# Kernel optimization log

Measured on AMD Instinct MI355X. Metric: run time of the kernel, lower is better.

## Reference

```python
import jax, jax.numpy as jnp
import numpy as np

INPUT_DIM = 4096
HIDDEN_DIMS = [2048, 1024, 512]
OUTPUT_DIM = 2
LAYER_DIMS = [INPUT_DIM] + HIDDEN_DIMS + [OUTPUT_DIM]
LAYER_IDX = np.concatenate([[0], np.cumsum(LAYER_DIMS)]).astype(int).tolist()
TOTAL_NODES = LAYER_IDX[-1]
FAN_IN = 128
BATCH = 512
EPS = 1e-5


def setup_inputs() -> dict:
    # Layered edge topology: each node in layer i receives FAN_IN random edges
    # from layer i-1 (matches how BINN uses set_connections).
    rng = np.random.default_rng(0)
    srcs, tgts = [], []
    for i in range(1, len(LAYER_DIMS)):
        ps, pe = LAYER_IDX[i - 1], LAYER_IDX[i]
        s, e = LAYER_IDX[i], LAYER_IDX[i + 1]
        dim = e - s
        srcs.append(rng.integers(ps, pe, size=(dim, FAN_IN)).reshape(-1))
        tgts.append(np.repeat(np.arange(s, e), FAN_IN))
    edge_src = jnp.asarray(np.concatenate(srcs), jnp.int32)
    edge_tgt = jnp.asarray(np.concatenate(tgts), jnp.int32)
    E = edge_src.shape[0]

    key = jax.random.key(0)
    kx, kw = jax.random.split(key)
    x = jax.random.normal(kx, (BATCH, INPUT_DIM), jnp.float32)
    # weight = randn(E) * 1/sqrt(fan_in)  (fan_in is FAN_IN for every target)
    weight = jax.random.normal(kw, (E,), jnp.float32) * (1.0 / np.sqrt(FAN_IN))
    bias = jnp.zeros((TOTAL_NODES - INPUT_DIM,), jnp.float32)
    n_hidden = sum(HIDDEN_DIMS)
    ln_gamma = jnp.ones((n_hidden,), jnp.float32)
    ln_beta = jnp.zeros((n_hidden,), jnp.float32)
    return dict(x=x, weight=weight, bias=bias, ln_gamma=ln_gamma,
                ln_beta=ln_beta, edge_src=edge_src, edge_tgt=edge_tgt)


def reference(x, weight, bias, ln_gamma, ln_beta, edge_src, edge_tgt):
    # activations held as [total_nodes, B] so segment_sum scatters on axis 0
    B = x.shape[0]
    acts = jnp.zeros((TOTAL_NODES, B), x.dtype).at[:INPUT_DIM].set(x.T)
    n_layers = len(LAYER_DIMS)
    for i in range(1, n_layers):  # fixed small layer count
        # full sparse mm over ALL edges each layer (faithful to original)
        contrib = weight[:, None] * acts[edge_src]            # [E, B]
        ws = jax.ops.segment_sum(contrib, edge_tgt,
                                 num_segments=TOTAL_NODES)    # [N, B]
        s, e = LAYER_IDX[i], LAYER_IDX[i + 1]
        cur = ws[s:e] + bias[s - INPUT_DIM:e - INPUT_DIM, None]
        if i < n_layers - 1:
            hs, he = s - INPUT_DIM, e - INPUT_DIM
            mean = jnp.mean(cur, axis=0, keepdims=True)
            var = jnp.var(cur, axis=0, keepdims=True)  # biased, as torch LN
            cur = (ln_gamma[hs:he, None] * (cur - mean) * jax.lax.rsqrt(var + EPS)
                   + ln_beta[hs:he, None])
            cur = jax.nn.relu(cur)
        acts = acts.at[s:e].set(cur)
    return acts[LAYER_IDX[-2]:LAYER_IDX[-1]].T  # [B, output_dim]
```

## Files before the change

### kernel.cpp

```cpp
#include <hip/hip_runtime.h>

#define BATCH 512
#define FAN_IN 128
#define EPS 1e-5f

typedef unsigned short u16;
typedef unsigned int u32;
typedef _Float16 f16;
typedef __attribute__((ext_vector_type(8))) short short8;
typedef __attribute__((ext_vector_type(4))) float f32x4;
typedef __attribute__((ext_vector_type(4))) _Float16 f16x4;

__device__ __forceinline__ u16 f2bf(float f) {
    union { float f; u32 u; } v; v.f = f;
    u32 r = v.u + 0x7fffu + ((v.u >> 16) & 1u);
    return (u16)(r >> 16);
}
__device__ __forceinline__ void ld16(const void* g, void* l) {
    __builtin_amdgcn_global_load_lds(
        (const __attribute__((address_space(1))) u32*)g,
        (__attribute__((address_space(3))) u32*)l, 16, 0, 0);
}

__device__ __forceinline__ void densify_node(
    float* row, int Kin, int ebase, int srcbase, u16* outrow,
    const float* __restrict__ weight, const int* __restrict__ edge_src) {
    const int t = threadIdx.x;
    for (int k = t; k < Kin; k += 256) row[k] = 0.f;
    __syncthreads();
    if (t < FAN_IN)
        atomicAdd(&row[edge_src[ebase + t] - srcbase], weight[ebase + t]);
    __syncthreads();
    for (int k0 = t * 8; k0 < Kin; k0 += 2048) {
        u16 pk[8];
#pragma unroll
        for (int i = 0; i < 8; ++i) pk[i] = f2bf(row[k0 + i]);
        *(uint4*)(outrow + k0) = *(const uint4*)pk;
    }
}

__global__ __launch_bounds__(256) void prep(
    const float* __restrict__ weight, const int* __restrict__ edge_src,
    const float* __restrict__ x, u16* __restrict__ Wd, u16* __restrict__ xb) {
    __shared__ float row[4096];
    const int bid = blockIdx.x, t = threadIdx.x;
    if (bid < 2048) {
        densify_node(row, 4096, bid * 128, 0, Wd + (size_t)bid * 4096,
                     weight, edge_src);
    } else {
        const int b = bid - 2048;
        const float* xr = x + (size_t)b * 4096;
        u16* xo = xb + (size_t)b * 4096;
        for (int k0 = t * 8; k0 < 4096; k0 += 2048) {
            const float4 f0 = *(const float4*)(xr + k0);
            const float4 f1 = *(const float4*)(xr + k0 + 4);
            uint4 pk;
            pk.x = f2bf(f0.x) | ((u32)f2bf(f0.y) << 16);
            pk.y = f2bf(f0.z) | ((u32)f2bf(f0.w) << 16);
            pk.z = f2bf(f1.x) | ((u32)f2bf(f1.y) << 16);
            pk.w = f2bf(f1.z) | ((u32)f2bf(f1.w) << 16);
            *(uint4*)(xo + k0) = pk;
        }
    }
}

__device__ __forceinline__ void gemm_body(
    u16* SM, int m_t, int n_t, int z, const u16* __restrict__ Act,
    const u16* __restrict__ W, f16* __restrict__ Cz, int M, int K,
    int kchunk) {
    u16* sA = SM;
    u16* sB = SM + 4096;
    const int tid = threadIdx.x;
    const int m0 = m_t * 64, n0 = n_t * 64, kbase = z * kchunk;
    f16* Cp = Cz + (size_t)z * BATCH * M;

    const int r = tid >> 2, c = tid & 3;
    const int q = c ^ ((r ^ (r >> 2)) & 3);
    const u16* gA = Act + (size_t)(n0 + r) * K + kbase + q * 8;
    const u16* gB = W + (size_t)(m0 + r) * K + kbase + q * 8;
    const int lo = tid * 8;

    const int wave = tid >> 6, lane = tid & 63;
    const int l15 = lane & 15, quad = lane >> 4;
    const int aoff = (wave & 1) * 32, boff = (wave >> 1) * 32;
    int offA[2], offB[2];
#pragma unroll
    for (int i = 0; i < 2; ++i) {
        const int ra = aoff + i * 16 + l15;
        offA[i] = ra * 32 + ((quad ^ ((ra ^ (ra >> 2)) & 3)) * 8);
        const int rb = boff + i * 16 + l15;
        offB[i] = rb * 32 + ((quad ^ ((rb ^ (rb >> 2)) & 3)) * 8);
    }

    f32x4 acc[2][2] = {};
    const int niter = kchunk >> 5;
    ld16(gA, &sA[lo]); ld16(gB, &sB[lo]);
    for (int it = 0; it < niter; ++it) {
        __syncthreads();
        if (it + 1 < niter) {
            const int k0 = (it + 1) << 5;
            const int nb = ((it + 1) & 1) * 2048;
            ld16(gA + k0, &sA[nb + lo]); ld16(gB + k0, &sB[nb + lo]);
        }
        const u16* a = sA + (it & 1) * 2048;
        const u16* b = sB + (it & 1) * 2048;
        const short8 a0 = *(const short8*)(a + offA[0]);
        const short8 a1 = *(const short8*)(a + offA[1]);
        const short8 b0 = *(const short8*)(b + offB[0]);
        const short8 b1 = *(const short8*)(b + offB[1]);
        acc[0][0] = __builtin_amdgcn_mfma_f32_16x16x32_bf16(a0, b0, acc[0][0], 0, 0, 0);
        acc[0][1] = __builtin_amdgcn_mfma_f32_16x16x32_bf16(a0, b1, acc[0][1], 0, 0, 0);
        acc[1][0] = __builtin_amdgcn_mfma_f32_16x16x32_bf16(a1, b0, acc[1][0], 0, 0, 0);
        acc[1][1] = __builtin_amdgcn_mfma_f32_16x16x32_bf16(a1, b1, acc[1][1], 0, 0, 0);
    }
#pragma unroll
    for (int i = 0; i < 2; ++i) {
        const int nb = n_t * 64 + aoff + i * 16 + quad * 4;
#pragma unroll
        for (int rr = 0; rr < 4; ++rr)
#pragma unroll
            for (int j = 0; j < 2; ++j) {
                const int mg = m0 + boff + j * 16 + l15;
                Cp[(size_t)(nb + rr) * M + mg] = (f16)acc[i][j][rr];
            }
    }
}

__device__ __forceinline__ void gemm128_body(
    u16* SM, int m_t, int n_t, int z, const u16* __restrict__ Act,
    const u16* __restrict__ W, f16* __restrict__ Cz, int M, int K,
    int kchunk) {
    u16* sA = SM;
    u16* sB = SM + 8192;
    const int tid = threadIdx.x;
    const int m0 = m_t * 128, n0 = n_t * 128, kbase = z * kchunk;
    f16* Cp = Cz + (size_t)z * BATCH * M;

    const int r = tid >> 2, c = tid & 3;
    const int q1 = c ^ ((r ^ (r >> 2)) & 3);
    const int r2 = r + 64;
    const int q2 = c ^ ((r2 ^ (r2 >> 2)) & 3);
    const u16* gA1 = Act + (size_t)(n0 + r) * K + kbase + q1 * 8;
    const u16* gA2 = Act + (size_t)(n0 + r2) * K + kbase + q2 * 8;
    const u16* gB1 = W + (size_t)(m0 + r) * K + kbase + q1 * 8;
    const u16* gB2 = W + (size_t)(m0 + r2) * K + kbase + q2 * 8;
    const int lo1 = tid * 8, lo2 = tid * 8 + 2048;

    const int wave = tid >> 6, lane = tid & 63;
    const int l15 = lane & 15, quad = lane >> 4;
    const int wn = (wave & 1) * 64, wm = (wave >> 1) * 64;
    int offA[4], offB[4];
#pragma unroll
    for (int i = 0; i < 4; ++i) {
        const int na = wn + i * 16 + l15;
        offA[i] = na * 32 + ((quad ^ ((na ^ (na >> 2)) & 3)) * 8);
        const int mb = wm + i * 16 + l15;
        offB[i] = mb * 32 + ((quad ^ ((mb ^ (mb >> 2)) & 3)) * 8);
    }

    f32x4 acc[4][4] = {};
    const int niter = kchunk >> 5;
    ld16(gA1, &sA[lo1]); ld16(gA2, &sA[lo2]);
    ld16(gB1, &sB[lo1]); ld16(gB2, &sB[lo2]);
    for (int it = 0; it < niter; ++it) {
        __syncthreads();
        if (it + 1 < niter) {
            const int k0 = (it + 1) << 5;
            const int nb = ((it + 1) & 1) * 4096;
            ld16(gA1 + k0, &sA[nb + lo1]); ld16(gA2 + k0, &sA[nb + lo2]);
            ld16(gB1 + k0, &sB[nb + lo1]); ld16(gB2 + k0, &sB[nb + lo2]);
        }
        const u16* a = sA + (it & 1) * 4096;
        const u16* b = sB + (it & 1) * 4096;
        short8 av[4], bv[4];
#pragma unroll
        for (int i = 0; i < 4; ++i) av[i] = *(const short8*)(a + offA[i]);
#pragma unroll
        for (int j = 0; j < 4; ++j) bv[j] = *(const short8*)(b + offB[j]);
#pragma unroll
        for (int i = 0; i < 4; ++i)
#pragma unroll
            for (int j = 0; j < 4; ++j)
                acc[i][j] = __builtin_amdgcn_mfma_f32_16x16x32_bf16(
                    av[i], bv[j], acc[i][j], 0, 0, 0);
    }
#pragma unroll
    for (int i = 0; i < 4; ++i) {
        const int nb = n0 + wn + i * 16 + quad * 4;
#pragma unroll
        for (int rr = 0; rr < 4; ++rr)
#pragma unroll
            for (int j = 0; j < 4; ++j) {
                const int mg = m0 + wm + j * 16 + l15;
                Cp[(size_t)(nb + rr) * M + mg] = (f16)acc[i][j][rr];
            }
    }
}

__global__ __launch_bounds__(256) void g1d(
    const u16* __restrict__ xb, u16* __restrict__ Wd, f16* __restrict__ Cz1,
    const float* __restrict__ weight, const int* __restrict__ edge_src) {
    __shared__ u16 SM[16384];
    const int bid = blockIdx.x;
    if (bid < 512) {
        gemm128_body(SM, bid & 15, (bid >> 4) & 3, bid >> 6, xb, Wd, Cz1,
                     2048, 4096, 512);
    } else if (bid < 1536) {
        const int u = bid - 512;
        densify_node((float*)SM, 2048, 262144 + u * 128, 4096,
                     Wd + 8388608 + (size_t)u * 2048, weight, edge_src);
    } else {
        const int u = bid - 1536;
        densify_node((float*)SM, 1024, 393216 + u * 128, 6144,
                     Wd + 10485760 + (size_t)u * 1024, weight, edge_src);
    }
}

__global__ __launch_bounds__(256, 8) void gemm_bt(
    const u16* __restrict__ Act, const u16* __restrict__ W,
    f16* __restrict__ Cz, int M, int K, int kchunk) {
    __shared__ u16 SM[8192];
    gemm_body(SM, blockIdx.x, blockIdx.y, blockIdx.z, Act, W, Cz, M, K, kchunk);
}

template <int M, int Z, bool WOUT>
__global__ __launch_bounds__(256) void fin(
    const f16* __restrict__ Cz, const float* __restrict__ bias_l,
    const float* __restrict__ gamma_l, const float* __restrict__ beta_l,
    u16* __restrict__ actb, const float* __restrict__ weight,
    const int* __restrict__ edge_src, const float* __restrict__ obias,
    float* __restrict__ out) {
    __shared__ float rowL[M];
    __shared__ float red[8];
    __shared__ float mrs[2];
    __shared__ float w_s[256];
    __shared__ int   s_s[256];
    __shared__ float pr[256];

    const int n = blockIdx.x, t = threadIdx.x;
    const size_t zs = (size_t)BATCH * M;
    const f16* base = Cz + (size_t)n * M;

    if (WOUT) { w_s[t] = weight[458752 + t]; s_s[t] = edge_src[458752 + t] - 7168; }

    float sum = 0.f, sq = 0.f;
    for (int m = t * 4; m < M; m += 1024) {
        float4 v = *(const float4*)(bias_l + m);
#pragma unroll
        for (int z = 0; z < Z; ++z) {
            const f16x4 cv = *(const f16x4*)(base + (size_t)z * zs + m);
            v.x += (float)cv.x; v.y += (float)cv.y;
            v.z += (float)cv.z; v.w += (float)cv.w;
        }
        *(float4*)(rowL + m) = v;
        sum += v.x + v.y + v.z + v.w;
        sq += v.x * v.x + v.y * v.y + v.z * v.z + v.w * v.w;
    }
#pragma unroll
    for (int o = 32; o; o >>= 1) { sum += __shfl_down(sum, o); sq += __shfl_down(sq, o); }
    if ((t & 63) == 0) { red[(t >> 6) * 2] = sum; red[(t >> 6) * 2 + 1] = sq; }
    __syncthreads();
    if (t == 0) {
        const float s = red[0] + red[2] + red[4] + red[6];
        const float qq = red[1] + red[3] + red[5] + red[7];
        const float mean = s / (float)M;
        const float var = qq / (float)M - mean * mean;
        mrs[0] = mean; mrs[1] = rsqrtf(var + EPS);
    }
    __syncthreads();
    const float mean = mrs[0], rstd = mrs[1];

    for (int m = t * 4; m < M; m += 1024) {
        const float4 v = *(const float4*)(rowL + m);
        const float4 g = *(const float4*)(gamma_l + m);
        const float4 bt = *(const float4*)(beta_l + m);
        const float o0 = fmaxf(fmaf(g.x * (v.x - mean), rstd, bt.x), 0.f);
        const float o1 = fmaxf(fmaf(g.y * (v.y - mean), rstd, bt.y), 0.f);
        const float o2 = fmaxf(fmaf(g.z * (v.z - mean), rstd, bt.z), 0.f);
        const float o3 = fmaxf(fmaf(g.w * (v.w - mean), rstd, bt.w), 0.f);
        if (WOUT) {
            rowL[m + 0] = o0; rowL[m + 1] = o1; rowL[m + 2] = o2; rowL[m + 3] = o3;
        } else {
            u16 pk[4] = {f2bf(o0), f2bf(o1), f2bf(o2), f2bf(o3)};
            *(uint2*)(actb + (size_t)n * M + m) = *(const uint2*)pk;
        }
    }
    if (WOUT) {
        __syncthreads();
        pr[t] = w_s[t] * rowL[s_s[t]];
        __syncthreads();
        if (t < 2) {
            float s = 0.f;
            for (int k = 0; k < FAN_IN; ++k) s += pr[t * FAN_IN + k];
            out[(size_t)n * 2 + t] = s + obias[t];
        }
    }
}

extern "C" void kernel_launch(void* const* d_in, const int* in_sizes, int n_in,
                              void* d_out, int out_size, void* d_ws, size_t ws_size,
                              hipStream_t stream) {
    const float* x        = (const float*)d_in[0];
    const float* weight   = (const float*)d_in[1];
    const float* bias     = (const float*)d_in[2];
    const float* ln_gamma = (const float*)d_in[3];
    const float* ln_beta  = (const float*)d_in[4];
    const int*   edge_src = (const int*)d_in[5];
    float* out = (float*)d_out;

    f16* Cz1 = (f16*)d_ws;
    f16* Cz2 = Cz1 + (size_t)8 * 512 * 2048;
    f16* Cz3 = Cz2 + (size_t)4 * 512 * 1024;
    u16* xb    = (u16*)(Cz3 + (size_t)8 * 512 * 512);
    u16* actb1 = xb + (size_t)512 * 4096;
    u16* actb2 = actb1 + (size_t)512 * 2048;
    u16* Wd    = actb2 + (size_t)512 * 1024;

    prep<<<2560, 256, 0, stream>>>(weight, edge_src, x, Wd, xb);
    g1d<<<2048, 256, 0, stream>>>(xb, Wd, Cz1, weight, edge_src);
    fin<2048, 8, false><<<512, 256, 0, stream>>>(
        Cz1, bias, ln_gamma, ln_beta, actb1, nullptr, nullptr, nullptr, nullptr);
    gemm_bt<<<dim3(16, 8, 4), 256, 0, stream>>>(actb1, Wd + 8388608, Cz2,
                                                1024, 2048, 512);
    fin<1024, 4, false><<<512, 256, 0, stream>>>(
        Cz2, bias + 2048, ln_gamma + 2048, ln_beta + 2048, actb2,
        nullptr, nullptr, nullptr, nullptr);
    gemm_bt<<<dim3(8, 8, 8), 256, 0, stream>>>(actb2, Wd + 10485760, Cz3,
                                               512, 1024, 128);
    fin<512, 8, true><<<512, 256, 0, stream>>>(
        Cz3, bias + 3072, ln_gamma + 3072, ln_beta + 3072, nullptr,
        weight, edge_src, bias + 3584, out);
}
```

Baseline: 118.8 us.

## Replace densified GEMM pipeline with direct sparse gather and atomic LN stats

Drops per-call weight densification and dense bf16 MFMA GEMMs. Each layer now directly gathers FAN_IN source rows of a transposed bf16 activation matrix. Per-batch LayerNorm sums are accumulated with shared and global atomics, then applied in a separate kernel. The final output layer is fused with the last LN. This does far fewer FLOPs but depends on irregular gather bandwidth and on atomics.

```diff
diff --git a/kernel.cpp b/kernel.cpp
--- a/kernel.cpp
+++ b/kernel.cpp
@@ -6,295 +6,137 @@
 
 typedef unsigned short u16;
 typedef unsigned int u32;
-typedef _Float16 f16;
-typedef __attribute__((ext_vector_type(8))) short short8;
-typedef __attribute__((ext_vector_type(4))) float f32x4;
-typedef __attribute__((ext_vector_type(4))) _Float16 f16x4;
 
 __device__ __forceinline__ u16 f2bf(float f) {
     union { float f; u32 u; } v; v.f = f;
     u32 r = v.u + 0x7fffu + ((v.u >> 16) & 1u);
     return (u16)(r >> 16);
 }
-__device__ __forceinline__ void ld16(const void* g, void* l) {
-    __builtin_amdgcn_global_load_lds(
-        (const __attribute__((address_space(1))) u32*)g,
-        (__attribute__((address_space(3))) u32*)l, 16, 0, 0);
+__device__ __forceinline__ float bf2f(u16 h) {
+    union { u32 u; float f; } v; v.u = ((u32)h) << 16; return v.f;
 }
 
-__device__ __forceinline__ void densify_node(
-    float* row, int Kin, int ebase, int srcbase, u16* outrow,
-    const float* __restrict__ weight, const int* __restrict__ edge_src) {
-    const int t = threadIdx.x;
-    for (int k = t; k < Kin; k += 256) row[k] = 0.f;
+__global__ __launch_bounds__(256) void prepk(
+    const float* __restrict__ x, u16* __restrict__ xT,
+    float* __restrict__ stats) {
+    const int tid = threadIdx.x, bid = blockIdx.x;
+    if (bid == 512) {
+        for (int i = tid; i < 3072; i += 256) stats[i] = 0.f;
+        return;
+    }
+    __shared__ float T[64][65];
+    const int f0 = (bid & 63) * 64, b0 = (bid >> 6) * 64;
+    const int r = tid >> 4, c4 = (tid & 15) * 4;
+#pragma unroll
+    for (int rr = 0; rr < 4; ++rr) {
+        const int row = r + rr * 16;
+        const float4 v = *(const float4*)(x + (size_t)(b0 + row) * 4096 + f0 + c4);
+        T[row][c4] = v.x; T[row][c4 + 1] = v.y;
+        T[row][c4 + 2] = v.z; T[row][c4 + 3] = v.w;
+    }
     __syncthreads();
-    if (t < FAN_IN)
-        atomicAdd(&row[edge_src[ebase + t] - srcbase], weight[ebase + t]);
-    __syncthreads();
-    for (int k0 = t * 8; k0 < Kin; k0 += 2048) {
-        u16 pk[8];
 #pragma unroll
-        for (int i = 0; i < 8; ++i) pk[i] = f2bf(row[k0 + i]);
-        *(uint4*)(outrow + k0) = *(const uint4*)pk;
+    for (int half = 0; half < 2; ++half) {
+        const int fr = (tid >> 3) + half * 32;
+        const int bq = (tid & 7) * 8;
+        uint4 pk;
+        pk.x = (u32)f2bf(T[bq + 0][fr]) | ((u32)f2bf(T[bq + 1][fr]) << 16);
+        pk.y = (u32)f2bf(T[bq + 2][fr]) | ((u32)f2bf(T[bq + 3][fr]) << 16);
+        pk.z = (u32)f2bf(T[bq + 4][fr]) | ((u32)f2bf(T[bq + 5][fr]) << 16);
+        pk.w = (u32)f2bf(T[bq + 6][fr]) | ((u32)f2bf(T[bq + 7][fr]) << 16);
+        *(uint4*)(xT + (size_t)(f0 + fr) * 512 + b0 + bq) = pk;
     }
 }
 
-__global__ __launch_bounds__(256) void prep(
-    const float* __restrict__ weight, const int* __restrict__ edge_src,
-    const float* __restrict__ x, u16* __restrict__ Wd, u16* __restrict__ xb) {
-    __shared__ float row[4096];
-    const int bid = blockIdx.x, t = threadIdx.x;
-    if (bid < 2048) {
-        densify_node(row, 4096, bid * 128, 0, Wd + (size_t)bid * 4096,
-                     weight, edge_src);
-    } else {
-        const int b = bid - 2048;
-        const float* xr = x + (size_t)b * 4096;
-        u16* xo = xb + (size_t)b * 4096;
-        for (int k0 = t * 8; k0 < 4096; k0 += 2048) {
-            const float4 f0 = *(const float4*)(xr + k0);
-            const float4 f1 = *(const float4*)(xr + k0 + 4);
-            uint4 pk;
-            pk.x = f2bf(f0.x) | ((u32)f2bf(f0.y) << 16);
-            pk.y = f2bf(f0.z) | ((u32)f2bf(f0.w) << 16);
-            pk.z = f2bf(f1.x) | ((u32)f2bf(f1.y) << 16);
-            pk.w = f2bf(f1.z) | ((u32)f2bf(f1.w) << 16);
-            *(uint4*)(xo + k0) = pk;
-        }
+template <int NT, int EBASE, int SRCBASE>
+__global__ __launch_bounds__(256) void gatherk(
+    const u16* __restrict__ srcAct, const float* __restrict__ weight,
+    const int* __restrict__ edge_src, const float* __restrict__ bias_l,
+    float* __restrict__ raw, float* __restrict__ gcs,
+    float* __restrict__ gcq) {
+    __shared__ float cs[256];
+    __shared__ float cq[256];
+    const int tid = threadIdx.x, bid = blockIdx.x;
+    const int rr = bid & 7, kk = bid >> 3;
+    const int bc = rr >> 2;
+    const int ng = kk * 4 + (rr & 3);
+    const int wave = __builtin_amdgcn_readfirstlane(tid >> 6);
+    const int lane = tid & 63;
+    const int node = ng * 4 + wave;
+    const u16* sb = srcAct + bc * 256 + lane * 4;
+    const int ebase = EBASE + node * FAN_IN;
+    float a0 = 0.f, a1 = 0.f, a2 = 0.f, a3 = 0.f;
+#pragma unroll 8
+    for (int k = 0; k < FAN_IN; ++k) {
+        const int src = edge_src[ebase + k] - SRCBASE;
+        const float w = weight[ebase + k];
+        const ushort4 v = *(const ushort4*)(sb + (size_t)src * 512);
+        a0 = fmaf(w, bf2f(v.x), a0);
+        a1 = fmaf(w, bf2f(v.y), a1);
+        a2 = fmaf(w, bf2f(v.z), a2);
+        a3 = fmaf(w, bf2f(v.w), a3);
+    }
+    const float bv = bias_l[node];
+    a0 += bv; a1 += bv; a2 += bv; a3 += bv;
+    float4 o; o.x = a0; o.y = a1; o.z = a2; o.w = a3;
+    *(float4*)(raw + (size_t)node * 512 + bc * 256 + lane * 4) = o;
+
+    cs[tid] = 0.f; cq[tid] = 0.f;
+    __syncthreads();
+    const int lb = lane * 4;
+    atomicAdd(&cs[lb + 0], a0); atomicAdd(&cq[lb + 0], a0 * a0);
+    atomicAdd(&cs[lb + 1], a1); atomicAdd(&cq[lb + 1], a1 * a1);
+    atomicAdd(&cs[lb + 2], a2); atomicAdd(&cq[lb + 2], a2 * a2);
+    atomicAdd(&cs[lb + 3], a3); atomicAdd(&cq[lb + 3], a3 * a3);
+    __syncthreads();
+    atomicAdd(&gcs[bc * 256 + tid], cs[tid]);
+    atomicAdd(&gcq[bc * 256 + tid], cq[tid]);
+}
+
+template <int M>
+__global__ __launch_bounds__(256) void lnapplyk(
+    const float* __restrict__ raw, const float* __restrict__ gcs,
+    const float* __restrict__ gcq, const float* __restrict__ gamma_l,
+    const float* __restrict__ beta_l, u16* __restrict__ actT) {
+    const int tid = threadIdx.x;
+    const int b0 = tid * 2;
+    const float inv = 1.f / (float)M;
+    const float m0 = gcs[b0] * inv, m1 = gcs[b0 + 1] * inv;
+    const float r0 = rsqrtf(gcq[b0] * inv - m0 * m0 + EPS);
+    const float r1 = rsqrtf(gcq[b0 + 1] * inv - m1 * m1 + EPS);
+    for (int row = blockIdx.x; row < M; row += 256) {
+        const float2 v = *(const float2*)(raw + (size_t)row * 512 + b0);
+        const float g = gamma_l[row], bt = beta_l[row];
+        const float o0 = fmaxf(fmaf(g * (v.x - m0), r0, bt), 0.f);
+        const float o1 = fmaxf(fmaf(g * (v.y - m1), r1, bt), 0.f);
+        *(u32*)(actT + (size_t)row * 512 + b0) =
+            (u32)f2bf(o0) | ((u32)f2bf(o1) << 16);
     }
 }
 
-__device__ __forceinline__ void gemm_body(
-    u16* SM, int m_t, int n_t, int z, const u16* __restrict__ Act,
-    const u16* __restrict__ W, f16* __restrict__ Cz, int M, int K,
-    int kchunk) {
-    u16* sA = SM;
-    u16* sB = SM + 4096;
-    const int tid = threadIdx.x;
-    const int m0 = m_t * 64, n0 = n_t * 64, kbase = z * kchunk;
-    f16* Cp = Cz + (size_t)z * BATCH * M;
-
-    const int r = tid >> 2, c = tid & 3;
-    const int q = c ^ ((r ^ (r >> 2)) & 3);
-    const u16* gA = Act + (size_t)(n0 + r) * K + kbase + q * 8;
-    const u16* gB = W + (size_t)(m0 + r) * K + kbase + q * 8;
-    const int lo = tid * 8;
-
-    const int wave = tid >> 6, lane = tid & 63;
-    const int l15 = lane & 15, quad = lane >> 4;
-    const int aoff = (wave & 1) * 32, boff = (wave >> 1) * 32;
-    int offA[2], offB[2];
-#pragma unroll
-    for (int i = 0; i < 2; ++i) {
-        const int ra = aoff + i * 16 + l15;
-        offA[i] = ra * 32 + ((quad ^ ((ra ^ (ra >> 2)) & 3)) * 8);
-        const int rb = boff + i * 16 + l15;
-        offB[i] = rb * 32 + ((quad ^ ((rb ^ (rb >> 2)) & 3)) * 8);
+__global__ __launch_bounds__(256) void outk(
+    const float* __restrict__ raw3, const float* __restrict__ gcs,
+    const float* __restrict__ gcq, const float* __restrict__ weight,
+    const int* __restrict__ edge_src, const float* __restrict__ gamma_l,
+    const float* __restrict__ beta_l, const float* __restrict__ bias_o,
+    float* __restrict__ out) {
+    const int tid = threadIdx.x, bid = blockIdx.x;
+    const int tgt = __builtin_amdgcn_readfirstlane(tid >> 7);
+    const int b = bid * 128 + (tid & 127);
+    const float inv = 1.f / 512.f;
+    const float mb = gcs[b] * inv;
+    const float rb = rsqrtf(gcq[b] * inv - mb * mb + EPS);
+    const int ebase = 458752 + tgt * FAN_IN;
+    float acc = 0.f;
+#pragma unroll 8
+    for (int k = 0; k < FAN_IN; ++k) {
+        const int src = edge_src[ebase + k] - 7168;
+        const float w = weight[ebase + k];
+        const float g = gamma_l[src], bt = beta_l[src];
+        const float v = raw3[(size_t)src * 512 + b];
+        acc = fmaf(w, fmaxf(fmaf(g * (v - mb), rb, bt), 0.f), acc);
     }
-
-    f32x4 acc[2][2] = {};
-    const int niter = kchunk >> 5;
-    ld16(gA, &sA[lo]); ld16(gB, &sB[lo]);
-    for (int it = 0; it < niter; ++it) {
-        __syncthreads();
-        if (it + 1 < niter) {
-            const int k0 = (it + 1) << 5;
-            const int nb = ((it + 1) & 1) * 2048;
-            ld16(gA + k0, &sA[nb + lo]); ld16(gB + k0, &sB[nb + lo]);
-        }
-        const u16* a = sA + (it & 1) * 2048;
-        const u16* b = sB + (it & 1) * 2048;
-        const short8 a0 = *(const short8*)(a + offA[0]);
-        const short8 a1 = *(const short8*)(a + offA[1]);
-        const short8 b0 = *(const short8*)(b + offB[0]);
-        const short8 b1 = *(const short8*)(b + offB[1]);
-        acc[0][0] = __builtin_amdgcn_mfma_f32_16x16x32_bf16(a0, b0, acc[0][0], 0, 0, 0);
-        acc[0][1] = __builtin_amdgcn_mfma_f32_16x16x32_bf16(a0, b1, acc[0][1], 0, 0, 0);
-        acc[1][0] = __builtin_amdgcn_mfma_f32_16x16x32_bf16(a1, b0, acc[1][0], 0, 0, 0);
-        acc[1][1] = __builtin_amdgcn_mfma_f32_16x16x32_bf16(a1, b1, acc[1][1], 0, 0, 0);
-    }
-#pragma unroll
-    for (int i = 0; i < 2; ++i) {
-        const int nb = n_t * 64 + aoff + i * 16 + quad * 4;
-#pragma unroll
-        for (int rr = 0; rr < 4; ++rr)
-#pragma unroll
-            for (int j = 0; j < 2; ++j) {
-                const int mg = m0 + boff + j * 16 + l15;
-                Cp[(size_t)(nb + rr) * M + mg] = (f16)acc[i][j][rr];
-            }
-    }
-}
-
-__device__ __forceinline__ void gemm128_body(
-    u16* SM, int m_t, int n_t, int z, const u16* __restrict__ Act,
-    const u16* __restrict__ W, f16* __restrict__ Cz, int M, int K,
-    int kchunk) {
-    u16* sA = SM;
-    u16* sB = SM + 8192;
-    const int tid = threadIdx.x;
-    const int m0 = m_t * 128, n0 = n_t * 128, kbase = z * kchunk;
-    f16* Cp = Cz + (size_t)z * BATCH * M;
-
-    const int r = tid >> 2, c = tid & 3;
-    const int q1 = c ^ ((r ^ (r >> 2)) & 3);
-    const int r2 = r + 64;
-    const int q2 = c ^ ((r2 ^ (r2 >> 2)) & 3);
-    const u16* gA1 = Act + (size_t)(n0 + r) * K + kbase + q1 * 8;
-    const u16* gA2 = Act + (size_t)(n0 + r2) * K + kbase + q2 * 8;
-    const u16* gB1 = W + (size_t)(m0 + r) * K + kbase + q1 * 8;
-    const u16* gB2 = W + (size_t)(m0 + r2) * K + kbase + q2 * 8;
-    const int lo1 = tid * 8, lo2 = tid * 8 + 2048;
-
-    const int wave = tid >> 6, lane = tid & 63;
-    const int l15 = lane & 15, quad = lane >> 4;
-    const int wn = (wave & 1) * 64, wm = (wave >> 1) * 64;
-    int offA[4], offB[4];
-#pragma unroll
-    for (int i = 0; i < 4; ++i) {
-        const int na = wn + i * 16 + l15;
-        offA[i] = na * 32 + ((quad ^ ((na ^ (na >> 2)) & 3)) * 8);
-        const int mb = wm + i * 16 + l15;
-        offB[i] = mb * 32 + ((quad ^ ((mb ^ (mb >> 2)) & 3)) * 8);
-    }
-
-    f32x4 acc[4][4] = {};
-    const int niter = kchunk >> 5;
-    ld16(gA1, &sA[lo1]); ld16(gA2, &sA[lo2]);
-    ld16(gB1, &sB[lo1]); ld16(gB2, &sB[lo2]);
-    for (int it = 0; it < niter; ++it) {
-        __syncthreads();
-        if (it + 1 < niter) {
-            const int k0 = (it + 1) << 5;
-            const int nb = ((it + 1) & 1) * 4096;
-            ld16(gA1 + k0, &sA[nb + lo1]); ld16(gA2 + k0, &sA[nb + lo2]);
-            ld16(gB1 + k0, &sB[nb + lo1]); ld16(gB2 + k0, &sB[nb + lo2]);
-        }
-        const u16* a = sA + (it & 1) * 4096;
-        const u16* b = sB + (it & 1) * 4096;
-        short8 av[4], bv[4];
-#pragma unroll
-        for (int i = 0; i < 4; ++i) av[i] = *(const short8*)(a + offA[i]);
-#pragma unroll
-        for (int j = 0; j < 4; ++j) bv[j] = *(const short8*)(b + offB[j]);
-#pragma unroll
-        for (int i = 0; i < 4; ++i)
-#pragma unroll
-            for (int j = 0; j < 4; ++j)
-                acc[i][j] = __builtin_amdgcn_mfma_f32_16x16x32_bf16(
-                    av[i], bv[j], acc[i][j], 0, 0, 0);
-    }
-#pragma unroll
-    for (int i = 0; i < 4; ++i) {
-        const int nb = n0 + wn + i * 16 + quad * 4;
-#pragma unroll
-        for (int rr = 0; rr < 4; ++rr)
-#pragma unroll
-            for (int j = 0; j < 4; ++j) {
-                const int mg = m0 + wm + j * 16 + l15;
-                Cp[(size_t)(nb + rr) * M + mg] = (f16)acc[i][j][rr];
-            }
-    }
-}
-
-__global__ __launch_bounds__(256) void g1d(
-    const u16* __restrict__ xb, u16* __restrict__ Wd, f16* __restrict__ Cz1,
-    const float* __restrict__ weight, const int* __restrict__ edge_src) {
-    __shared__ u16 SM[16384];
-    const int bid = blockIdx.x;
-    if (bid < 512) {
-        gemm128_body(SM, bid & 15, (bid >> 4) & 3, bid >> 6, xb, Wd, Cz1,
-                     2048, 4096, 512);
-    } else if (bid < 1536) {
-        const int u = bid - 512;
-        densify_node((float*)SM, 2048, 262144 + u * 128, 4096,
-                     Wd + 8388608 + (size_t)u * 2048, weight, edge_src);
-    } else {
-        const int u = bid - 1536;
-        densify_node((float*)SM, 1024, 393216 + u * 128, 6144,
-                     Wd + 10485760 + (size_t)u * 1024, weight, edge_src);
-    }
-}
-
-__global__ __launch_bounds__(256, 8) void gemm_bt(
-    const u16* __restrict__ Act, const u16* __restrict__ W,
-    f16* __restrict__ Cz, int M, int K, int kchunk) {
-    __shared__ u16 SM[8192];
-    gemm_body(SM, blockIdx.x, blockIdx.y, blockIdx.z, Act, W, Cz, M, K, kchunk);
-}
-
-template <int M, int Z, bool WOUT>
-__global__ __launch_bounds__(256) void fin(
-    const f16* __restrict__ Cz, const float* __restrict__ bias_l,
-    const float* __restrict__ gamma_l, const float* __restrict__ beta_l,
-    u16* __restrict__ actb, const float* __restrict__ weight,
-    const int* __restrict__ edge_src, const float* __restrict__ obias,
-    float* __restrict__ out) {
-    __shared__ float rowL[M];
-    __shared__ float red[8];
-    __shared__ float mrs[2];
-    __shared__ float w_s[256];
-    __shared__ int   s_s[256];
-    __shared__ float pr[256];
-
-    const int n = blockIdx.x, t = threadIdx.x;
-    const size_t zs = (size_t)BATCH * M;
-    const f16* base = Cz + (size_t)n * M;
-
-    if (WOUT) { w_s[t] = weight[458752 + t]; s_s[t] = edge_src[458752 + t] - 7168; }
-
-    float sum = 0.f, sq = 0.f;
-    for (int m = t * 4; m < M; m += 1024) {
-        float4 v = *(const float4*)(bias_l + m);
-#pragma unroll
-        for (int z = 0; z < Z; ++z) {
-            const f16x4 cv = *(const f16x4*)(base + (size_t)z * zs + m);
-            v.x += (float)cv.x; v.y += (float)cv.y;
-            v.z += (float)cv.z; v.w += (float)cv.w;
-        }
-        *(float4*)(rowL + m) = v;
-        sum += v.x + v.y + v.z + v.w;
-        sq += v.x * v.x + v.y * v.y + v.z * v.z + v.w * v.w;
-    }
-#pragma unroll
-    for (int o = 32; o; o >>= 1) { sum += __shfl_down(sum, o); sq += __shfl_down(sq, o); }
-    if ((t & 63) == 0) { red[(t >> 6) * 2] = sum; red[(t >> 6) * 2 + 1] = sq; }
-    __syncthreads();
-    if (t == 0) {
-        const float s = red[0] + red[2] + red[4] + red[6];
-        const float qq = red[1] + red[3] + red[5] + red[7];
-        const float mean = s / (float)M;
-        const float var = qq / (float)M - mean * mean;
-        mrs[0] = mean; mrs[1] = rsqrtf(var + EPS);
-    }
-    __syncthreads();
-    const float mean = mrs[0], rstd = mrs[1];
-
-    for (int m = t * 4; m < M; m += 1024) {
-        const float4 v = *(const float4*)(rowL + m);
-        const float4 g = *(const float4*)(gamma_l + m);
-        const float4 bt = *(const float4*)(beta_l + m);
-        const float o0 = fmaxf(fmaf(g.x * (v.x - mean), rstd, bt.x), 0.f);
-        const float o1 = fmaxf(fmaf(g.y * (v.y - mean), rstd, bt.y), 0.f);
-        const float o2 = fmaxf(fmaf(g.z * (v.z - mean), rstd, bt.z), 0.f);
-        const float o3 = fmaxf(fmaf(g.w * (v.w - mean), rstd, bt.w), 0.f);
-        if (WOUT) {
-            rowL[m + 0] = o0; rowL[m + 1] = o1; rowL[m + 2] = o2; rowL[m + 3] = o3;
-        } else {
-            u16 pk[4] = {f2bf(o0), f2bf(o1), f2bf(o2), f2bf(o3)};
-            *(uint2*)(actb + (size_t)n * M + m) = *(const uint2*)pk;
-        }
-    }
-    if (WOUT) {
-        __syncthreads();
-        pr[t] = w_s[t] * rowL[s_s[t]];
-        __syncthreads();
-        if (t < 2) {
-            float s = 0.f;
-            for (int k = 0; k < FAN_IN; ++k) s += pr[t * FAN_IN + k];
-            out[(size_t)n * 2 + t] = s + obias[t];
-        }
-    }
+    out[(size_t)b * 2 + tgt] = acc + bias_o[tgt];
 }
 
 extern "C" void kernel_launch(void* const* d_in, const int* in_sizes, int n_in,
@@ -308,26 +150,26 @@
     const int*   edge_src = (const int*)d_in[5];
     float* out = (float*)d_out;
 
-    f16* Cz1 = (f16*)d_ws;
-    f16* Cz2 = Cz1 + (size_t)8 * 512 * 2048;
-    f16* Cz3 = Cz2 + (size_t)4 * 512 * 1024;
-    u16* xb    = (u16*)(Cz3 + (size_t)8 * 512 * 512);
-    u16* actb1 = xb + (size_t)512 * 4096;
-    u16* actb2 = actb1 + (size_t)512 * 2048;
-    u16* Wd    = actb2 + (size_t)512 * 1024;
+    u16* xT    = (u16*)d_ws;
+    u16* actT1 = xT + (size_t)4096 * 512;
+    u16* actT2 = actT1 + (size_t)2048 * 512;
+    float* raw1 = (float*)(actT2 + (size_t)1024 * 512);
+    float* raw2 = raw1 + (size_t)2048 * 512;
+    float* raw3 = raw2 + (size_t)1024 * 512;
+    float* stats = raw3 + (size_t)512 * 512;
 
-    prep<<<2560, 256, 0, stream>>>(weight, edge_src, x, Wd, xb);
-    g1d<<<2048, 256, 0, stream>>>(xb, Wd, Cz1, weight, edge_src);
-    fin<2048, 8, false><<<512, 256, 0, stream>>>(
-        Cz1, bias, ln_gamma, ln_beta, actb1, nullptr, nullptr, nullptr, nullptr);
-    gemm_bt<<<dim3(16, 8, 4), 256, 0, stream>>>(actb1, Wd + 8388608, Cz2,
-                                                1024, 2048, 512);
-    fin<1024, 4, false><<<512, 256, 0, stream>>>(
-        Cz2, bias + 2048, ln_gamma + 2048, ln_beta + 2048, actb2,
-        nullptr, nullptr, nullptr, nullptr);
-    gemm_bt<<<dim3(8, 8, 8), 256, 0, stream>>>(actb2, Wd + 10485760, Cz3,
-                                               512, 1024, 128);
-    fin<512, 8, true><<<512, 256, 0, stream>>>(
-        Cz3, bias + 3072, ln_gamma + 3072, ln_beta + 3072, nullptr,
-        weight, edge_src, bias + 3584, out);
+    prepk<<<513, 256, 0, stream>>>(x, xT, stats);
+    gatherk<2048, 0, 0><<<1024, 256, 0, stream>>>(
+        xT, weight, edge_src, bias, raw1, stats, stats + 512);
+    lnapplyk<2048><<<256, 256, 0, stream>>>(
+        raw1, stats, stats + 512, ln_gamma, ln_beta, actT1);
+    gatherk<1024, 262144, 4096><<<512, 256, 0, stream>>>(
+        actT1, weight, edge_src, bias + 2048, raw2, stats + 1024, stats + 1536);
+    lnapplyk<1024><<<256, 256, 0, stream>>>(
+        raw2, stats + 1024, stats + 1536, ln_gamma + 2048, ln_beta + 2048, actT2);
+    gatherk<512, 393216, 6144><<<256, 256, 0, stream>>>(
+        actT2, weight, edge_src, bias + 3072, raw3, stats + 2048, stats + 2560);
+    outk<<<4, 256, 0, stream>>>(
+        raw3, stats + 2048, stats + 2560, weight, edge_src,
+        ln_gamma + 3072, ln_beta + 3072, bias + 3584, out);
 }
```

Result: slower. 158.7 us (+33.6%).
